# Optimization experiments

Hardware: AMD Instinct MI355X
Metric: run time of the kernel (lower is better)

## Reference

```python
import jax, jax.numpy as jnp
import numpy as np

N_HEAD = 12
N_EMBD = 768
HEAD_DIM = N_EMBD // N_HEAD
B, S = 4, 2048


def setup_inputs() -> dict:
    key = jax.random.key(0)
    k1, k2, k3, k4, k5 = jax.random.split(key, 5)
    x = jax.random.normal(k1, (B, S, N_EMBD), dtype=jnp.float32)
    # causal additive mask: 1.0 where attention is disallowed (strictly upper triangle)
    mask = (1.0 - jnp.tril(jnp.ones((S, S), dtype=jnp.float32)))[None, None, :, :]
    scale = 0.02
    W_attn = jax.random.normal(k2, (N_EMBD, 3 * N_EMBD), dtype=jnp.float32) * scale
    b_attn = jnp.zeros((3 * N_EMBD,), dtype=jnp.float32)
    W_proj = jax.random.normal(k3, (N_EMBD, N_EMBD), dtype=jnp.float32) * scale
    b_proj = jnp.zeros((N_EMBD,), dtype=jnp.float32)
    return {"x": x, "mask": mask, "W_attn": W_attn, "b_attn": b_attn,
            "W_proj": W_proj, "b_proj": b_proj}


def reference(x, mask, W_attn, b_attn, W_proj, b_proj):
    Bn, Sn, _ = x.shape
    qkv = x @ W_attn + b_attn                      # [B,S,3E]
    q, k, v = jnp.split(qkv, 3, axis=-1)           # each [B,S,E]

    def heads(t):
        return t.reshape(Bn, Sn, N_HEAD, HEAD_DIM).transpose(0, 2, 1, 3)  # [B,H,S,D]

    q, k, v = heads(q), heads(k), heads(v)
    attn = jnp.einsum('bhqd,bhkd->bhqk', q, k) / jnp.sqrt(jnp.float32(HEAD_DIM))
    attn = attn + mask * (-1e9)
    attn = jax.nn.softmax(attn, axis=-1)
    # dropout in inference mode = identity
    out = jnp.einsum('bhqk,bhkd->bhqd', attn, v)   # [B,H,S,D]
    out = out.transpose(0, 2, 1, 3).reshape(Bn, Sn, N_EMBD)
    return out @ W_proj + b_proj
```

## Files before the change

### kernel.cpp

```cpp
#include <hip/hip_runtime.h>
#include <stdint.h>

#define NHEAD 12
#define HDIM  64
#define EMB   768
#define N3    2304
#define SEQ   2048
#define BATCH 4
#define MROWS 8192

#define QSCALE 0.18033688011112042f

typedef __bf16 bf16_t;
typedef __bf16 bf16x8 __attribute__((ext_vector_type(8)));
typedef __bf16 bf16x4 __attribute__((ext_vector_type(4)));
typedef short  s16x4  __attribute__((ext_vector_type(4)));
typedef float  f32x4  __attribute__((ext_vector_type(4)));

__device__ __forceinline__ void gld_lds16(void* lds, const void* g) {
    __builtin_amdgcn_global_load_lds((const __attribute__((address_space(1))) void*)g,
                                     (__attribute__((address_space(3))) void*)lds,
                                     16, 0, 0);
}

__device__ __forceinline__ float fast_exp2(float x) {
    return __builtin_amdgcn_exp2f(x);
}

__device__ __forceinline__ f32x4 mfma16_bf16(bf16x4 a, bf16x4 b, f32x4 c) {
#if __has_builtin(__builtin_amdgcn_mfma_f32_16x16x16_bf16)
    return __builtin_amdgcn_mfma_f32_16x16x16_bf16(a, b, c, 0, 0, 0);
#else
    union U { bf16x4 h; s16x4 s; };
    U ua, ub; ua.h = a; ub.h = b;
    return __builtin_amdgcn_mfma_f32_16x16x16bf16_1k(ua.s, ub.s, c, 0, 0, 0);
#endif
}

__global__ __launch_bounds__(256) void prep_kernel(
    const float* __restrict__ Wa, bf16_t* __restrict__ WaT,
    const float* __restrict__ Wp, bf16_t* __restrict__ WpT,
    const float* __restrict__ x,  bf16_t* __restrict__ xb)
{
    __shared__ float tile[32][33];
    const int bid = blockIdx.x;
    if (bid < 2304) {
        const float* W; bf16_t* WT; int K, N, b;
        if (bid < 1728) { W = Wa; WT = WaT; K = 768; N = 2304; b = bid; }
        else            { W = Wp; WT = WpT; K = 768; N = 768;  b = bid - 1728; }
        const int nb = N / 32;
        const int n0 = (b % nb) * 32, k0 = (b / nb) * 32;
        const int tx = threadIdx.x & 31, ty = threadIdx.x >> 5;
#pragma unroll
        for (int i = 0; i < 32; i += 8)
            tile[ty + i][tx] = W[(size_t)(k0 + ty + i) * N + (n0 + tx)];
        __syncthreads();
#pragma unroll
        for (int i = 0; i < 32; i += 8)
            WT[(size_t)(n0 + ty + i) * K + (k0 + tx)] = (bf16_t)tile[tx][ty + i];
    } else {
        const int n8 = MROWS * EMB / 8;
        int idx    = (bid - 2304) * 256 + threadIdx.x;
        const int stride = 1536 * 256;
        for (int i = idx; i < n8; i += stride) {
            float4 a = ((const float4*)x)[i * 2];
            float4 b = ((const float4*)x)[i * 2 + 1];
            bf16x8 v;
            v[0] = (bf16_t)a.x; v[1] = (bf16_t)a.y; v[2] = (bf16_t)a.z; v[3] = (bf16_t)a.w;
            v[4] = (bf16_t)b.x; v[5] = (bf16_t)b.y; v[6] = (bf16_t)b.z; v[7] = (bf16_t)b.w;
            ((bf16x8*)xb)[i] = v;
        }
    }
}

template<int MODE>
__global__ __launch_bounds__(256) void gemm_kernel(
    const bf16_t* __restrict__ Av,
    const bf16_t* __restrict__ BT,
    const float* __restrict__ bias,
    float* __restrict__ out,
    bf16_t* __restrict__ qbuf,
    bf16_t* __restrict__ kbuf,
    bf16_t* __restrict__ vbuf,
    int Ncols)
{
    const int K = 768;
    __shared__ alignas(16) bf16_t As[2][128 * 32];
    __shared__ alignas(16) bf16_t Bs[2][128 * 32];

    const int tid    = threadIdx.x;
    const int wave   = tid >> 6;
    const int lane   = tid & 63;
    const int lane15 = lane & 15;
    const int quad   = lane >> 4;

    const int bid   = blockIdx.x;
    const int chunk = (int)(gridDim.x >> 3);
    const int swz   = (bid & 7) * chunk + (bid >> 3);
    const int NB    = Ncols >> 7;
    const int mBase = (swz / NB) * 128;
    const int nBase = (swz % NB) * 128;

    const int wm = (wave >> 1) * 64;
    const int wn = (wave & 1) * 64;

    f32x4 acc[4][4];
#pragma unroll
    for (int i = 0; i < 4; i++)
#pragma unroll
        for (int j = 0; j < 4; j++) acc[i][j] = (f32x4){0.f, 0.f, 0.f, 0.f};

    const bf16_t* aSrc = Av + (size_t)mBase * K;
    const bf16_t* bSrc = BT + (size_t)nBase * K;

    const int srow = lane >> 2;
    const int sch  = lane & 3;

    auto issueA = [&](int k0, int buf) {
#pragma unroll
        for (int p = 0; p < 2; p++) {
            int r0  = p * 64 + wave * 16;
            int row = r0 + srow;
            int lch = sch ^ (row & 3);
            gld_lds16(&As[buf][r0 * 32], aSrc + (size_t)row * K + k0 + lch * 8);
        }
    };
    auto issueB = [&](int k0, int buf) {
#pragma unroll
        for (int p = 0; p < 2; p++) {
            int r0  = p * 64 + wave * 16;
            int row = r0 + srow;
            int lch = sch ^ (row & 3);
            gld_lds16(&Bs[buf][r0 * 32], bSrc + (size_t)row * K + k0 + lch * 8);
        }
    };

    issueA(0, 0);
    issueB(0, 0);

    for (int k0 = 0, it = 0; k0 < K; k0 += 32, it++) {
        const int buf = it & 1;
        __syncthreads();
        if (k0 + 32 < K) {
            issueB(k0 + 32, buf ^ 1);
            issueA(k0 + 32, buf ^ 1);
        }

        bf16x8 aF[4], bF[4];
#pragma unroll
        for (int t = 0; t < 4; t++) {
            int ra = wm + t * 16 + lane15;
            int rb = wn + t * 16 + lane15;
            aF[t] = *(const bf16x8*)&As[buf][ra * 32 + (quad ^ (ra & 3)) * 8];
            bF[t] = *(const bf16x8*)&Bs[buf][rb * 32 + (quad ^ (rb & 3)) * 8];
        }
#pragma unroll
        for (int i = 0; i < 4; i++)
#pragma unroll
            for (int j = 0; j < 4; j++)
                acc[i][j] = __builtin_amdgcn_mfma_f32_16x16x32_bf16(aF[i], bF[j], acc[i][j], 0, 0, 0);
    }

    const int region = nBase / EMB;
#pragma unroll
    for (int i = 0; i < 4; i++) {
#pragma unroll
        for (int j = 0; j < 4; j++) {
            int gn = nBase + wn + j * 16 + lane15;
            float bv = bias[gn];
            if (region == 2) {
                int within = gn - 2 * EMB;
                int h = within >> 6, d = within & 63;
                int gm0 = mBase + wm + i * 16 + quad * 4;
                int b = gm0 >> 11, s = gm0 & 2047;
                int bh = b * NHEAD + h;
                bf16x4 v4;
#pragma unroll
                for (int r = 0; r < 4; r++) v4[r] = (bf16_t)(acc[i][j][r] + bv);
                *(bf16x4*)&vbuf[((size_t)bh * HDIM + d) * SEQ + s] = v4;
            } else {
                bf16_t* dst = (region == 0) ? qbuf : kbuf;
                const float scale = (region == 0) ? QSCALE : 1.0f;
                int within = gn - region * EMB;
                int h = within >> 6, d = within & 63;
#pragma unroll
                for (int r = 0; r < 4; r++) {
                    int gm = mBase + wm + i * 16 + quad * 4 + r;
                    int b = gm >> 11, s = gm & 2047;
                    int bh = b * NHEAD + h;
                    dst[((size_t)bh * SEQ + s) * HDIM + d] = (bf16_t)((acc[i][j][r] + bv) * scale);
                }
            }
        }
    }
}

__global__ __launch_bounds__(256) void proj_kernel(
    const bf16_t* __restrict__ Av,
    const bf16_t* __restrict__ BT,
    const float*  __restrict__ bias,
    float* __restrict__ out)
{
    const int K = 768;
    __shared__ alignas(16) bf16_t As[2][64 * 64];
    __shared__ alignas(16) bf16_t Bs[2][128 * 64];

    const int tid    = threadIdx.x;
    const int wave   = tid >> 6;
    const int lane   = tid & 63;
    const int lane15 = lane & 15;
    const int quad   = lane >> 4;

    const int bid   = blockIdx.x;
    const int swz   = (bid & 7) * 96 + (bid >> 3);
    const int mBase = (swz / 6) * 64;
    const int nBase = (swz % 6) * 128;

    f32x4 acc[4][2];
#pragma unroll
    for (int t = 0; t < 4; t++)
#pragma unroll
        for (int u = 0; u < 2; u++) acc[t][u] = (f32x4){0.f, 0.f, 0.f, 0.f};

    const bf16_t* aSrc = Av + (size_t)mBase * K;
    const bf16_t* bSrc = BT + (size_t)nBase * K;

    const int srow8 = lane >> 3;
    const int sch8  = lane & 7;

    auto issueA = [&](int k0, int buf) {
#pragma unroll
        for (int p = 0; p < 2; p++) {
            int r0  = wave * 8 + p * 32;
            int row = r0 + srow8;
            int lch = sch8 ^ (row & 7);
            gld_lds16(&As[buf][r0 * 64], aSrc + (size_t)row * K + k0 + lch * 8);
        }
    };
    auto issueB = [&](int k0, int buf) {
#pragma unroll
        for (int p = 0; p < 4; p++) {
            int r0  = wave * 8 + p * 32;
            int row = r0 + srow8;
            int lch = sch8 ^ (row & 7);
            gld_lds16(&Bs[buf][r0 * 64], bSrc + (size_t)row * K + k0 + lch * 8);
        }
    };

    issueA(0, 0);
    issueB(0, 0);

    for (int k0 = 0, it = 0; k0 < K; k0 += 64, it++) {
        const int buf = it & 1;
        __syncthreads();
        if (k0 + 64 < K) {
            issueB(k0 + 64, buf ^ 1);
            issueA(k0 + 64, buf ^ 1);
        }

        bf16x8 aF[2][4], bF[2][2];
#pragma unroll
        for (int kk = 0; kk < 2; kk++) {
#pragma unroll
            for (int t = 0; t < 4; t++) {
                int ra = t * 16 + lane15;
                aF[kk][t] = *(const bf16x8*)&As[buf][ra * 64 + (((quad + kk * 4) ^ (ra & 7)) * 8)];
            }
#pragma unroll
            for (int u = 0; u < 2; u++) {
                int rb = wave * 32 + u * 16 + lane15;
                bF[kk][u] = *(const bf16x8*)&Bs[buf][rb * 64 + (((quad + kk * 4) ^ (rb & 7)) * 8)];
            }
        }
#pragma unroll
        for (int kk = 0; kk < 2; kk++)
#pragma unroll
            for (int t = 0; t < 4; t++)
#pragma unroll
                for (int u = 0; u < 2; u++)
                    acc[t][u] = __builtin_amdgcn_mfma_f32_16x16x32_bf16(aF[kk][t], bF[kk][u], acc[t][u], 0, 0, 0);
    }

#pragma unroll
    for (int t = 0; t < 4; t++) {
#pragma unroll
        for (int u = 0; u < 2; u++) {
            int gn = nBase + wave * 32 + u * 16 + lane15;
            float bv = bias[gn];
#pragma unroll
            for (int r = 0; r < 4; r++) {
                int gm = mBase + t * 16 + quad * 4 + r;
                out[(size_t)gm * EMB + gn] = acc[t][u][r] + bv;
            }
        }
    }
}

__global__ __launch_bounds__(256) void attn_kernel(
    const bf16_t* __restrict__ qbuf,
    const bf16_t* __restrict__ kbuf,
    const bf16_t* __restrict__ vtbuf,
    bf16_t* __restrict__ obuf)
{
    __shared__ alignas(16) bf16_t Ks[2][64 * 64];
    __shared__ alignas(16) bf16_t Vs[2][64 * 64];
    __shared__ alignas(16) bf16_t Plds[4][16 * 72];

    const int tid    = threadIdx.x;
    const int wave   = tid >> 6;
    const int lane   = tid & 63;
    const int lane15 = lane & 15;
    const int quad   = lane >> 4;

    const int bid = blockIdx.x;
    const int swz = (bid & 7) * 96 + (bid >> 3);
    const int bh = swz >> 4;
    const int j  = swz & 15;

    const bf16_t* Qp = qbuf  + (size_t)bh * SEQ * HDIM;
    const bf16_t* Kp = kbuf  + (size_t)bh * SEQ * HDIM;
    const bf16_t* Vp = vtbuf + (size_t)bh * HDIM * SEQ;
    bf16_t* pl = &Plds[wave][0];
    const int b = bh / NHEAD, h = bh % NHEAD;

    const int srow8 = lane >> 3;
    const int sch8  = lane & 7;

    auto issueKV = [&](int kb, int buf) {
#pragma unroll
        for (int p = 0; p < 2; p++) {
            int r0  = p * 32 + wave * 8;
            int row = r0 + srow8;
            int lch = sch8 ^ (row & 7);
            gld_lds16(&Ks[buf][r0 * 64], Kp + (size_t)(kb + row) * HDIM + lch * 8);
            gld_lds16(&Vs[buf][r0 * 64], Vp + (size_t)row * SEQ + kb + lch * 8);
        }
    };

    for (int seg = 0; seg < 2; seg++) {
        const int qt = seg ? (31 - j) : j;
        const int q0 = qt * 64 + wave * 16;

        const bf16x8 qf0 = *(const bf16x8*)&Qp[(size_t)(q0 + lane15) * HDIM + quad * 8];
        const bf16x8 qf1 = *(const bf16x8*)&Qp[(size_t)(q0 + lane15) * HDIM + 32 + quad * 8];

        float lrow = 0.f;
        f32x4 oT[4];
#pragma unroll
        for (int t = 0; t < 4; t++) oT[t] = (f32x4){0.f, 0.f, 0.f, 0.f};

        const int nT = qt + 1;
        __syncthreads();
        issueKV(0, 0);

        for (int kt = 0; kt < nT; kt++) {
            const int buf = kt & 1;
            __syncthreads();
            if (kt + 1 < nT) issueKV((kt + 1) * 64, buf ^ 1);

            const int kb = kt * 64;

            f32x4 sT[4];
            __builtin_amdgcn_s_setprio(1);
#pragma unroll
            for (int kg = 0; kg < 4; kg++) {
                sT[kg] = (f32x4){0.f, 0.f, 0.f, 0.f};
                int row = kg * 16 + lane15;
                bf16x8 kf0 = *(const bf16x8*)&Ks[buf][row * 64 + ((quad    ) ^ (row & 7)) * 8];
                bf16x8 kf1 = *(const bf16x8*)&Ks[buf][row * 64 + ((quad + 4) ^ (row & 7)) * 8];
                sT[kg] = __builtin_amdgcn_mfma_f32_16x16x32_bf16(kf0, qf0, sT[kg], 0, 0, 0);
                sT[kg] = __builtin_amdgcn_mfma_f32_16x16x32_bf16(kf1, qf1, sT[kg], 0, 0, 0);
            }
            __builtin_amdgcn_s_setprio(0);

            if (kb + 64 > q0) {
                const int query = q0 + lane15;
#pragma unroll
                for (int kg = 0; kg < 4; kg++) {
                    int key0 = kb + kg * 16 + quad * 4;
#pragma unroll
                    for (int r = 0; r < 4; r++)
                        sT[kg][r] = (key0 + r <= query) ? sT[kg][r] : -1e30f;
                }
            }

            bf16x4 pf[4];
#pragma unroll
            for (int kg = 0; kg < 4; kg++) {
#pragma unroll
                for (int r = 0; r < 4; r++) sT[kg][r] = fast_exp2(sT[kg][r]);
                lrow += (sT[kg][0] + sT[kg][1]) + (sT[kg][2] + sT[kg][3]);
                bf16x4 v;
#pragma unroll
                for (int r = 0; r < 4; r++) v[r] = (bf16_t)sT[kg][r];
                pf[kg] = v;
            }

            __builtin_amdgcn_s_setprio(1);
#pragma unroll
            for (int t = 0; t < 4; t++) {
                int vrow = t * 16 + lane15;
#pragma unroll
                for (int kg = 0; kg < 4; kg++) {
                    int c    = kg * 2 + (quad >> 1);
                    int phys = c ^ (vrow & 7);
                    bf16x4 vf = *(const bf16x4*)&Vs[buf][vrow * 64 + phys * 8 + (quad & 1) * 4];
                    oT[t] = mfma16_bf16(vf, pf[kg], oT[t]);
                }
            }
            __builtin_amdgcn_s_setprio(0);
        }

        lrow += __shfl_xor(lrow, 16, 64);
        lrow += __shfl_xor(lrow, 32, 64);
        const float inv = 1.0f / lrow;

#pragma unroll
        for (int t = 0; t < 4; t++)
#pragma unroll
            for (int r = 0; r < 4; r++)
                pl[lane15 * 72 + t * 16 + quad * 4 + r] = (bf16_t)(oT[t][r] * inv);

        const int qrow = lane >> 2;
        const int ch   = lane & 3;
        bf16_t* orow = &obuf[((size_t)(b * SEQ + q0 + qrow)) * EMB + h * HDIM];
#pragma unroll
        for (int p = 0; p < 2; p++) {
            bf16x8 v = *(const bf16x8*)&pl[qrow * 72 + (ch + p * 4) * 8];
            *(bf16x8*)&orow[(ch + p * 4) * 8] = v;
        }
    }
}

extern "C" void kernel_launch(void* const* d_in, const int* in_sizes, int n_in,
                              void* d_out, int out_size, void* d_ws, size_t ws_size,
                              hipStream_t stream) {
    const float* x      = (const float*)d_in[0];
    const float* W_attn = (const float*)d_in[2];
    const float* b_attn = (const float*)d_in[3];
    const float* W_proj = (const float*)d_in[4];
    const float* b_proj = (const float*)d_in[5];
    float* out = (float*)d_out;

    bf16_t* ws  = (bf16_t*)d_ws;
    bf16_t* WaT = ws;
    bf16_t* WpT = WaT + (size_t)N3 * EMB;
    bf16_t* Qb  = WpT + (size_t)EMB * EMB;
    bf16_t* Kb  = Qb + (size_t)BATCH * NHEAD * SEQ * HDIM;
    bf16_t* Vt  = Kb + (size_t)BATCH * NHEAD * SEQ * HDIM;
    bf16_t* Ob  = Vt + (size_t)BATCH * NHEAD * SEQ * HDIM;
    bf16_t* xb  = Ob;

    prep_kernel<<<3840, 256, 0, stream>>>(W_attn, WaT, W_proj, WpT, x, xb);

    gemm_kernel<1><<<1152, 256, 0, stream>>>(
        xb, WaT, b_attn, nullptr, Qb, Kb, Vt, N3);

    attn_kernel<<<BATCH * NHEAD * 16, 256, 0, stream>>>(Qb, Kb, Vt, Ob);

    proj_kernel<<<768, 256, 0, stream>>>(Ob, WpT, b_proj, out);
}
```

Baseline: 218.1 us.

## Use 128-query tiles per block with two 16-row sub-tiles per wave, heaviest first

The attention kernel moves from blocks that each handle a pair of 64-query tiles (balanced causal pairs) to one 128-query tile per block. Each wave now handles 32 queries as two 16-row sub-tiles, so every K/V tile loaded into LDS serves twice as many queries and the number of K/V tile loads drops. Blocks are ordered so the longest causal tiles run first, which replaces the paired balancing scheme. The cost is more registers per wave and per-block work that now varies with query position. Sub-tiles lying entirely above the diagonal are skipped.

```diff
diff --git a/kernel.cpp b/kernel.cpp
--- a/kernel.cpp
+++ b/kernel.cpp
@@ -313,9 +313,9 @@
     const int quad   = lane >> 4;
 
     const int bid = blockIdx.x;
-    const int swz = (bid & 7) * 96 + (bid >> 3);
-    const int bh = swz >> 4;
-    const int j  = swz & 15;
+    const int idx = bid >> 3;
+    const int qt  = 15 - idx / 6;
+    const int bh  = (bid & 7) * 6 + idx % 6;
 
     const bf16_t* Qp = qbuf  + (size_t)bh * SEQ * HDIM;
     const bf16_t* Kp = kbuf  + (size_t)bh * SEQ * HDIM;
@@ -337,28 +337,37 @@
         }
     };
 
-    for (int seg = 0; seg < 2; seg++) {
-        const int qt = seg ? (31 - j) : j;
-        const int q0 = qt * 64 + wave * 16;
-
-        const bf16x8 qf0 = *(const bf16x8*)&Qp[(size_t)(q0 + lane15) * HDIM + quad * 8];
-        const bf16x8 qf1 = *(const bf16x8*)&Qp[(size_t)(q0 + lane15) * HDIM + 32 + quad * 8];
-
-        float lrow = 0.f;
-        f32x4 oT[4];
-#pragma unroll
-        for (int t = 0; t < 4; t++) oT[t] = (f32x4){0.f, 0.f, 0.f, 0.f};
-
-        const int nT = qt + 1;
+    const int q0w = qt * 128 + wave * 32;
+
+    bf16x8 qf[2][2];
+#pragma unroll
+    for (int qq = 0; qq < 2; qq++) {
+        const int q0q = q0w + qq * 16;
+        qf[qq][0] = *(const bf16x8*)&Qp[(size_t)(q0q + lane15) * HDIM + quad * 8];
+        qf[qq][1] = *(const bf16x8*)&Qp[(size_t)(q0q + lane15) * HDIM + 32 + quad * 8];
+    }
+
+    float lrow[2] = {0.f, 0.f};
+    f32x4 oT[2][4];
+#pragma unroll
+    for (int qq = 0; qq < 2; qq++)
+#pragma unroll
+        for (int t = 0; t < 4; t++) oT[qq][t] = (f32x4){0.f, 0.f, 0.f, 0.f};
+
+    const int nT = 2 * qt + 2;
+    issueKV(0, 0);
+
+    for (int kt = 0; kt < nT; kt++) {
+        const int buf = kt & 1;
         __syncthreads();
-        issueKV(0, 0);
-
-        for (int kt = 0; kt < nT; kt++) {
-            const int buf = kt & 1;
-            __syncthreads();
-            if (kt + 1 < nT) issueKV((kt + 1) * 64, buf ^ 1);
-
-            const int kb = kt * 64;
+        if (kt + 1 < nT) issueKV((kt + 1) * 64, buf ^ 1);
+
+        const int kb = kt * 64;
+
+#pragma unroll
+        for (int qq = 0; qq < 2; qq++) {
+            const int q0q = q0w + qq * 16;
+            if (kb > q0q + 15) continue;
 
             f32x4 sT[4];
             __builtin_amdgcn_s_setprio(1);
@@ -368,13 +377,13 @@
                 int row = kg * 16 + lane15;
                 bf16x8 kf0 = *(const bf16x8*)&Ks[buf][row * 64 + ((quad    ) ^ (row & 7)) * 8];
                 bf16x8 kf1 = *(const bf16x8*)&Ks[buf][row * 64 + ((quad + 4) ^ (row & 7)) * 8];
-                sT[kg] = __builtin_amdgcn_mfma_f32_16x16x32_bf16(kf0, qf0, sT[kg], 0, 0, 0);
-                sT[kg] = __builtin_amdgcn_mfma_f32_16x16x32_bf16(kf1, qf1, sT[kg], 0, 0, 0);
+                sT[kg] = __builtin_amdgcn_mfma_f32_16x16x32_bf16(kf0, qf[qq][0], sT[kg], 0, 0, 0);
+                sT[kg] = __builtin_amdgcn_mfma_f32_16x16x32_bf16(kf1, qf[qq][1], sT[kg], 0, 0, 0);
             }
             __builtin_amdgcn_s_setprio(0);
 
-            if (kb + 64 > q0) {
-                const int query = q0 + lane15;
+            if (kb + 64 > q0q) {
+                const int query = q0q + lane15;
 #pragma unroll
                 for (int kg = 0; kg < 4; kg++) {
                     int key0 = kb + kg * 16 + quad * 4;
@@ -389,7 +398,7 @@
             for (int kg = 0; kg < 4; kg++) {
 #pragma unroll
                 for (int r = 0; r < 4; r++) sT[kg][r] = fast_exp2(sT[kg][r]);
-                lrow += (sT[kg][0] + sT[kg][1]) + (sT[kg][2] + sT[kg][3]);
+                lrow[qq] += (sT[kg][0] + sT[kg][1]) + (sT[kg][2] + sT[kg][3]);
                 bf16x4 v;
 #pragma unroll
                 for (int r = 0; r < 4; r++) v[r] = (bf16_t)sT[kg][r];
@@ -405,25 +414,30 @@
                     int c    = kg * 2 + (quad >> 1);
                     int phys = c ^ (vrow & 7);
                     bf16x4 vf = *(const bf16x4*)&Vs[buf][vrow * 64 + phys * 8 + (quad & 1) * 4];
-                    oT[t] = mfma16_bf16(vf, pf[kg], oT[t]);
+                    oT[qq][t] = mfma16_bf16(vf, pf[kg], oT[qq][t]);
                 }
             }
             __builtin_amdgcn_s_setprio(0);
         }
-
-        lrow += __shfl_xor(lrow, 16, 64);
-        lrow += __shfl_xor(lrow, 32, 64);
-        const float inv = 1.0f / lrow;
+    }
+
+#pragma unroll
+    for (int qq = 0; qq < 2; qq++) {
+        const int q0q = q0w + qq * 16;
+        float l = lrow[qq];
+        l += __shfl_xor(l, 16, 64);
+        l += __shfl_xor(l, 32, 64);
+        const float inv = 1.0f / l;
 
 #pragma unroll
         for (int t = 0; t < 4; t++)
 #pragma unroll
             for (int r = 0; r < 4; r++)
-                pl[lane15 * 72 + t * 16 + quad * 4 + r] = (bf16_t)(oT[t][r] * inv);
+                pl[lane15 * 72 + t * 16 + quad * 4 + r] = (bf16_t)(oT[qq][t][r] * inv);
 
         const int qrow = lane >> 2;
         const int ch   = lane & 3;
-        bf16_t* orow = &obuf[((size_t)(b * SEQ + q0 + qrow)) * EMB + h * HDIM];
+        bf16_t* orow = &obuf[((size_t)(b * SEQ + q0q + qrow)) * EMB + h * HDIM];
 #pragma unroll
         for (int p = 0; p < 2; p++) {
             bf16x8 v = *(const bf16x8*)&pl[qrow * 72 + (ch + p * 4) * 8];
@@ -456,7 +470,7 @@
     gemm_kernel<1><<<1152, 256, 0, stream>>>(
         xb, WaT, b_attn, nullptr, Qb, Kb, Vt, N3);
 
-    attn_kernel<<<BATCH * NHEAD * 16, 256, 0, stream>>>(Qb, Kb, Vt, Ob);
+    attn_kernel<<<768, 256, 0, stream>>>(Qb, Kb, Vt, Ob);
 
     proj_kernel<<<768, 256, 0, stream>>>(Ob, WpT, b_proj, out);
 }
```

New measurement: 225.5 us. 1.03x slower.
